# Optimization experiments

Hardware: AMD Instinct MI355X
Metric: run time of the kernel (lower is better)

Reference implementation:

```python
import jax, jax.numpy as jnp
import numpy as np

N_ATOMS = 16384
N_BLOCKS = 4096
K = 3          # top-k nearest context atoms (min(3, n_ctx) in original; n_ctx >> 3 here)
EPS_W = 1e-8   # inverse-distance weight epsilon (matches original)
EPS_D = 1e-12  # tiny epsilon inside sqrt for numerical safety of the distance


def setup_inputs() -> dict:
    key = jax.random.key(0)
    k1, k2, k3, k4, k5 = jax.random.split(key, 5)
    # coordinates spread out like real molecular coords (Angstrom-ish scale)
    X = jax.random.normal(k1, (N_ATOMS, 3), dtype=jnp.float32) * 10.0
    base_noise = jax.random.normal(k2, (N_ATOMS, 3), dtype=jnp.float32)      # randn_like(X)
    centroid_noise = jax.random.normal(k3, (N_ATOMS, 3), dtype=jnp.float32)  # per-atom randn(3)
    block_ids = jnp.sort(jax.random.randint(k4, (N_ATOMS,), 0, N_BLOCKS)).astype(jnp.int32)
    generate_mask = jax.random.randint(k5, (N_BLOCKS,), 0, 2).astype(bool)
    return {
        "X": X,
        "base_noise": base_noise,
        "centroid_noise": centroid_noise,
        "block_ids": block_ids,
        "generate_mask": generate_mask,
    }


def reference(X, base_noise, centroid_noise, block_ids, generate_mask):
    """Vectorized sample_chemical_prior: for every generated atom, find the 3
    nearest CONTEXT atoms, take an inverse-distance-weighted centroid, and add
    0.5 * gaussian noise. Non-generated atoms keep base_noise (randn_like)."""
    n = X.shape[0]
    gen_atoms = generate_mask[block_ids]           # [N] atoms being generated
    ctx = ~gen_atoms                               # [N] context atoms

    # pairwise squared distances via ||a||^2 + ||b||^2 - 2 a.b  -> [N, N]
    xn = jnp.sum(X * X, axis=-1)
    sq = xn[:, None] + xn[None, :] - 2.0 * (X @ X.T)
    d = jnp.sqrt(jnp.maximum(sq, 0.0) + EPS_D)

    # only context atoms are valid neighbor candidates; exclude self for safety
    not_self = ~jnp.eye(n, dtype=bool)
    d = jnp.where(ctx[None, :] & not_self, d, jnp.inf)

    # k nearest context atoms per row (smallest distances)
    neg_dk, idx = jax.lax.top_k(-d, K)             # [N, K]
    dk = -neg_dk

    # inverse-distance weights, normalized (matches original)
    w = 1.0 / (dk + EPS_W)
    w = w / jnp.sum(w, axis=-1, keepdims=True)

    coords = X[idx]                                # [N, K, 3] gather neighbor coords
    centroid = jnp.sum(coords * w[..., None], axis=1)  # [N, 3]

    x0 = jnp.where(gen_atoms[:, None], centroid + 0.5 * centroid_noise, base_noise)
    return x0
```

## Files before the change

kernel.cpp:

```cpp
#include <hip/hip_runtime.h>
#include <cstdint>

#define N_ATOMS 16384
#define NBLK 64
#define NTHR 256
#define G 24
#define NCELLS 13824
#define NCELLS_PAD 14336
#define CPT 14
#define BOX_LO -48.0f
#define INV_CELL 0.25f
#define SINIT 3.0e38f

#define OFF_COUNTS 0
#define OFF_BLKGEN 256
#define OFF_BLKGOFF 512
#define OFF_FLAGS 1024
#define OFF_CNT 3072
#define OFF_START 60416
#define OFF_GENIDX 118016
#define OFF_CTX4 183552

__device__ __forceinline__ int cell1(float x) {
    int c = (int)floorf((x - BOX_LO) * INV_CELL);
    return min(max(c, 0), G - 1);
}

__device__ __forceinline__ void ins3(float v, int vi,
                                     float& s1, float& s2, float& s3,
                                     int& i1, int& i2, int& i3)
{
    const bool b1 = v < s1, b2 = v < s2, b3 = v < s3;
    s3 = b2 ? s2 : (b3 ? v : s3);   i3 = b2 ? i2 : (b3 ? vi : i3);
    s2 = b1 ? s1 : (b2 ? v : s2);   i2 = b1 ? i1 : (b2 ? vi : i2);
    s1 = b1 ? v : s1;               i1 = b1 ? vi : i1;
}

__device__ __forceinline__ void ins3v(float v, float& s1, float& s2, float& s3)
{
    const bool b1 = v < s1, b2 = v < s2, b3 = v < s3;
    s3 = b2 ? s2 : (b3 ? v : s3);
    s2 = b1 ? s1 : (b2 ? v : s2);
    s1 = b1 ? v : s1;
}

__global__ __launch_bounds__(256)
void k0_zero(int4* __restrict__ cell_cnt4)
{
    cell_cnt4[blockIdx.x * 256 + threadIdx.x] = make_int4(0, 0, 0, 0);
}

__global__ __launch_bounds__(NTHR)
void k1_classify(const float* __restrict__ X,
                 const int* __restrict__ block_ids,
                 const unsigned int* __restrict__ mask,
                 const float* __restrict__ base_noise,
                 float* __restrict__ out,
                 unsigned long long* __restrict__ flags,
                 int* __restrict__ blk_gen,
                 int* __restrict__ cell_cnt)
{
    __shared__ int sflag;
    __shared__ int wg[4];
    const int t = threadIdx.x;
    const int wave = t >> 6, lane = t & 63;

    if (t == 0) sflag = 0;
    __syncthreads();
    if (mask[t] > 1u) sflag = 1;
    __syncthreads();
    const bool is_u8 = (sflag != 0);
    const unsigned char* m8 = (const unsigned char*)mask;

    const int i = blockIdx.x * NTHR + t;
    const int bid = block_ids[i];
    const bool g = is_u8 ? (m8[bid] != 0) : (mask[bid] != 0u);

    out[3 * i + 0] = base_noise[3 * i + 0];
    out[3 * i + 1] = base_noise[3 * i + 1];
    out[3 * i + 2] = base_noise[3 * i + 2];

    const unsigned long long mg = __ballot(g);
    if (lane == 0) { flags[blockIdx.x * 4 + wave] = mg; wg[wave] = __popcll(mg); }
    __syncthreads();
    if (t == 0) blk_gen[blockIdx.x] = wg[0] + wg[1] + wg[2] + wg[3];

    if (!g) {
        const float x = X[3 * i], y = X[3 * i + 1], z = X[3 * i + 2];
        const int cx = cell1(x), cy = cell1(y), cz = cell1(z);
        atomicAdd(&cell_cnt[(cz * G + cy) * G + cx], 1);
    }
}

__global__ __launch_bounds__(1024)
void k2_scan(int* __restrict__ cell_cnt,
             int* __restrict__ cell_start,
             const int* __restrict__ blk_gen,
             int* __restrict__ blk_goff,
             int* __restrict__ counts)
{
    const int t = threadIdx.x;
    const int wave = t >> 6, lane = t & 63;
    int loc[CPT]; int sum = 0;
    #pragma unroll
    for (int k = 0; k < CPT; ++k) {
        const int v = cell_cnt[t * CPT + k];
        loc[k] = sum; sum += v;
    }
    int v = sum;
    #pragma unroll
    for (int d = 1; d < 64; d <<= 1) { const int u = __shfl_up(v, d); if (lane >= d) v += u; }
    __shared__ int wsum[16], wexc[16];
    if (lane == 63) wsum[wave] = v;
    __syncthreads();
    if (t < 16) {
        int v2 = wsum[t];
        const int orig = v2;
        #pragma unroll
        for (int d = 1; d < 16; d <<= 1) { const int u = __shfl_up(v2, d); if (t >= d) v2 += u; }
        wexc[t] = v2 - orig;
    }
    __syncthreads();
    const int base = wexc[wave] + (v - sum);
    #pragma unroll
    for (int k = 0; k < CPT; ++k) {
        cell_start[t * CPT + k] = base + loc[k];
        cell_cnt[t * CPT + k] = 0;
    }
    if (t == 1023) cell_start[NCELLS_PAD] = base + sum;
    __syncthreads();
    if (t < 64) {
        const int o = blk_gen[t];
        int s = o;
        #pragma unroll
        for (int d = 1; d < 64; d <<= 1) { const int u = __shfl_up(s, d); if (t >= d) s += u; }
        blk_goff[t] = s - o;
        if (t == 63) { counts[1] = s; counts[0] = N_ATOMS - s; }
    }
}

__global__ __launch_bounds__(NTHR)
void k3_scatter(const float* __restrict__ X,
                const unsigned long long* __restrict__ flags,
                const int* __restrict__ blk_goff,
                const int* __restrict__ cell_start,
                int* __restrict__ cell_cur,
                float4* __restrict__ ctx4s,
                int* __restrict__ genidx)
{
    const int t = threadIdx.x;
    const int wave = t >> 6, lane = t & 63;
    const int i = blockIdx.x * NTHR + t;
    const unsigned long long fw = flags[blockIdx.x * 4 + wave];
    const bool g = (fw >> lane) & 1ull;
    int og = blk_goff[blockIdx.x];
    int oc = blockIdx.x * NTHR - og;
    #pragma unroll
    for (int w = 0; w < 4; ++w) {
        if (w < wave) {
            const int p = __popcll(flags[blockIdx.x * 4 + w]);
            og += p; oc += 64 - p;
        }
    }
    const unsigned long long below = (1ull << lane) - 1ull;
    og += __popcll(fw & below);
    oc += __popcll((~fw) & below);
    if (g) {
        genidx[og] = i;
    } else {
        const float x = X[3 * i], y = X[3 * i + 1], z = X[3 * i + 2];
        float xn = x * x; xn += y * y; xn += z * z;
        const int cx = cell1(x), cy = cell1(y), cz = cell1(z);
        const int c = (cz * G + cy) * G + cx;
        const int pos = cell_start[c] + atomicAdd(&cell_cur[c], 1);
        ctx4s[pos] = make_float4(x, y, z, xn);
    }
}

__global__ __launch_bounds__(512)
void k4_search(const float* __restrict__ X,
               const float* __restrict__ cnoise,
               const int* __restrict__ counts,
               const int* __restrict__ cell_start,
               const float4* __restrict__ ctx4s,
               const int* __restrict__ genidx,
               float* __restrict__ out)
{
    const int n_gen = counts[1];
    const int wave = threadIdx.x >> 6, lane = threadIdx.x & 63;
    const int slot = (int)blockIdx.x * 8 + wave;
    if (slot >= n_gen) return;

    const int ai = genidx[slot];
    const float qx = X[3 * ai], qy = X[3 * ai + 1], qz = X[3 * ai + 2];
    float xnq = qx * qx; xnq += qy * qy; xnq += qz * qz;
    const int cqx = cell1(qx), cqy = cell1(qy), cqz = cell1(qz);

    float s1 = SINIT, s2 = SINIT, s3 = SINIT;
    int i1 = 0, i2 = 0, i3 = 0;

    auto searchOwner = [&](int ebase_r, int jc) -> int {
        int L = 0;
        #pragma unroll
        for (int stp = 32; stp >= 1; stp >>= 1) {
            const int cand = L + stp;
            const int bv = __shfl(ebase_r, cand);
            if (bv <= jc) L = cand;
        }
        return L;
    };

    auto flatScan = [&](int T, int ebase_r, int pk_r) {
        const int iters = (T + 63) >> 6;
        if (iters == 0) return;
        int jc0 = min(lane, T - 1);
        int p0 = __shfl(pk_r, searchOwner(ebase_r, jc0)) + jc0;
        float4 cc0 = ctx4s[p0];
        for (int it = 0; it < iters; ++it) {
            int p1 = p0; float4 cc1 = cc0;
            if (it + 1 < iters) {
                const int jc1 = min((it + 1) * 64 + lane, T - 1);
                p1 = __shfl(pk_r, searchOwner(ebase_r, jc1)) + jc1;
                cc1 = ctx4s[p1];
            }
            if (it * 64 + lane < T) {
                const float dot = qx * cc0.x + qy * cc0.y + qz * cc0.z;
                const float sq = (xnq + cc0.w) - 2.0f * dot;
                ins3(sq, p0, s1, s2, s3, i1, i2, i3);
            }
            p0 = p1; cc0 = cc1;
        }
    };

    auto prefixT = [&](int cnt, int& ebase_r, int& T) {
        int pre = cnt;
        #pragma unroll
        for (int d = 1; d < 64; d <<= 1) {
            const int u = __shfl_up(pre, d);
            if (lane >= d) pre += u;
        }
        T = __shfl(pre, 63);
        ebase_r = pre - cnt;
    };

    auto shellCell = [&](int r, int u, int S, int& st, int& cnt) {
        st = 0; cnt = 0;
        if (u < S) {
            const int B = 2 * r + 1, F = B * B, P8 = 8 * r;
            int dx, dy, dz;
            if (u < 2 * F) {
                dz = (u < F) ? -r : r;
                const int v = (u < F) ? u : u - F;
                dx = v % B - r; dy = v / B - r;
            } else {
                const int v = u - 2 * F;
                dz = v / P8 - (r - 1);
                const int w = v % P8;
                if (w < 2 * r)      { dx = -r + w;          dy = -r; }
                else if (w < 4 * r) { dx = r;               dy = -r + (w - 2 * r); }
                else if (w < 6 * r) { dx = r - (w - 4 * r); dy = r; }
                else                { dx = -r;              dy = r - (w - 6 * r); }
            }
            const int cx = cqx + dx, cy = cqy + dy, cz = cqz + dz;
            if ((unsigned)cx < G && (unsigned)cy < G && (unsigned)cz < G) {
                const int c = (cz * G + cy) * G + cx;
                st = cell_start[c];
                cnt = cell_start[c + 1] - st;
            }
        }
    };

    int cnt = 0, st = 0;
    if (lane < 27) {
        const int dx = lane % 3 - 1, dy = (lane / 3) % 3 - 1, dz = lane / 9 - 1;
        const int cx = cqx + dx, cy = cqy + dy, cz = cqz + dz;
        if ((unsigned)cx < G && (unsigned)cy < G && (unsigned)cz < G) {
            const int c = (cz * G + cy) * G + cx;
            st = cell_start[c];
            cnt = cell_start[c + 1] - st;
        }
    }
    int ebase, T;
    prefixT(cnt, ebase, T);
    flatScan(T, ebase, st - ebase);
    int C = T;
    bool dirty = (T > 0);
    float gm3 = SINIT;

    int r = 1;
    for (;;) {
        if (C >= 3) {
            if (dirty) {
                float m1 = s1, m2 = s2, m3 = s3;
                #pragma unroll
                for (int m = 1; m < 64; m <<= 1) {
                    const float a = __shfl_xor(m1, m);
                    const float b = __shfl_xor(m2, m);
                    const float c = __shfl_xor(m3, m);
                    ins3v(a, m1, m2, m3); ins3v(b, m1, m2, m3); ins3v(c, m1, m2, m3);
                }
                gm3 = m3; dirty = false;
            }
            const float bnd = (float)(4 * r) * (float)(4 * r);
            if (gm3 + 0.01f < bnd) break;
        }
        if (r >= G) break;
        ++r;
        const int S = 24 * r * r + 2;
        const int nro = (S + 63) >> 6;
        int st0, c0;
        shellCell(r, lane, S, st0, c0);
        for (int ro = 0; ro < nro; ++ro) {
            int st1 = st0, c1 = c0;
            if (ro + 1 < nro) shellCell(r, (ro + 1) * 64 + lane, S, st1, c1);
            int eb, Tr;
            prefixT(c0, eb, Tr);
            if (Tr > 0) {
                flatScan(Tr, eb, st0 - eb);
                C += Tr; dirty = true;
            }
            st0 = st1; c0 = c1;
        }
    }

    #pragma unroll
    for (int m = 1; m < 64; m <<= 1) {
        const float a = __shfl_xor(s1, m); const int ja = __shfl_xor(i1, m);
        const float b = __shfl_xor(s2, m); const int jb = __shfl_xor(i2, m);
        const float c = __shfl_xor(s3, m); const int jc = __shfl_xor(i3, m);
        ins3(a, ja, s1, s2, s3, i1, i2, i3);
        ins3(b, jb, s1, s2, s3, i1, i2, i3);
        ins3(c, jc, s1, s2, s3, i1, i2, i3);
    }

    if (lane == 0) {
        const float d1 = sqrtf(fmaxf(s1, 0.0f) + 1e-12f);
        const float d2 = sqrtf(fmaxf(s2, 0.0f) + 1e-12f);
        const float d3 = sqrtf(fmaxf(s3, 0.0f) + 1e-12f);
        float w1 = 1.0f / (d1 + 1e-8f);
        float w2 = 1.0f / (d2 + 1e-8f);
        float w3 = 1.0f / (d3 + 1e-8f);
        float wsum = w1 + w2;
        wsum += w3;
        w1 /= wsum; w2 /= wsum; w3 /= wsum;
        const float4 c1 = ctx4s[i1];
        const float4 c2 = ctx4s[i2];
        const float4 c3 = ctx4s[i3];
        float cxo = w1 * c1.x + w2 * c2.x; cxo += w3 * c3.x;
        float cyo = w1 * c1.y + w2 * c2.y; cyo += w3 * c3.y;
        float czo = w1 * c1.z + w2 * c2.z; czo += w3 * c3.z;
        out[3 * ai + 0] = cxo + 0.5f * cnoise[3 * ai + 0];
        out[3 * ai + 1] = cyo + 0.5f * cnoise[3 * ai + 1];
        out[3 * ai + 2] = czo + 0.5f * cnoise[3 * ai + 2];
    }
}

extern "C" void kernel_launch(void* const* d_in, const int* in_sizes, int n_in,
                              void* d_out, int out_size, void* d_ws, size_t ws_size,
                              hipStream_t stream) {
    const float* X          = (const float*)d_in[0];
    const float* base_noise = (const float*)d_in[1];
    const float* cnoise     = (const float*)d_in[2];
    const int*   block_ids  = (const int*)d_in[3];
    const unsigned int* gmask = (const unsigned int*)d_in[4];
    float* out = (float*)d_out;

    char* ws = (char*)d_ws;
    int*    counts     = (int*)(ws + OFF_COUNTS);
    int*    blk_gen    = (int*)(ws + OFF_BLKGEN);
    int*    blk_goff   = (int*)(ws + OFF_BLKGOFF);
    unsigned long long* flags = (unsigned long long*)(ws + OFF_FLAGS);
    int*    cell_cnt   = (int*)(ws + OFF_CNT);
    int*    cell_start = (int*)(ws + OFF_START);
    int*    genidx     = (int*)(ws + OFF_GENIDX);
    float4* ctx4s      = (float4*)(ws + OFF_CTX4);

    k0_zero<<<NCELLS_PAD / 1024, 256, 0, stream>>>((int4*)cell_cnt);
    k1_classify<<<NBLK, NTHR, 0, stream>>>(X, block_ids, gmask, base_noise,
                                           out, flags, blk_gen, cell_cnt);
    k2_scan<<<1, 1024, 0, stream>>>(cell_cnt, cell_start, blk_gen, blk_goff, counts);
    k3_scatter<<<NBLK, NTHR, 0, stream>>>(X, flags, blk_goff, cell_start,
                                          cell_cnt, ctx4s, genidx);
    k4_search<<<N_ATOMS / 8, 512, 0, stream>>>(X, cnoise, counts, cell_start,
                                               ctx4s, genidx, out);
}
```

Measured before the change: 52.24 us.

## Replace per-cell shell expansion with doubling-radius x-row segment scans

```diff
diff --git a/kernel.cpp b/kernel.cpp
--- a/kernel.cpp
+++ b/kernel.cpp
@@ -243,83 +243,77 @@
         ebase_r = pre - cnt;
     };
 
-    auto shellCell = [&](int r, int u, int S, int& st, int& cnt) {
-        st = 0; cnt = 0;
-        if (u < S) {
-            const int B = 2 * r + 1, F = B * B, P8 = 8 * r;
-            int dx, dy, dz;
-            if (u < 2 * F) {
-                dz = (u < F) ? -r : r;
-                const int v = (u < F) ? u : u - F;
-                dx = v % B - r; dy = v / B - r;
+    auto ringScan = [&](int P, int R) {
+        const int B = 2 * R + 1;
+        const int NR = B * B;
+        const int NS = 2 * NR;
+        auto segRange = [&](int u, int& st, int& cnt) {
+            st = 0; cnt = 0;
+            if (u >= NS) return;
+            const int side = (u >= NR) ? 1 : 0;
+            const int v = side ? u - NR : u;
+            const int dy = v % B - R, dz = v / B - R;
+            const int cy = cqy + dy, cz = cqz + dz;
+            if ((unsigned)cy >= G || (unsigned)cz >= G) return;
+            const bool inner = max(abs(dy), abs(dz)) <= P;
+            int xlo, xhi;
+            if (inner) {
+                if (side) { xlo = cqx + P + 1; xhi = cqx + R; }
+                else      { xlo = cqx - R;     xhi = cqx - P - 1; }
             } else {
-                const int v = u - 2 * F;
-                dz = v / P8 - (r - 1);
-                const int w = v % P8;
-                if (w < 2 * r)      { dx = -r + w;          dy = -r; }
-                else if (w < 4 * r) { dx = r;               dy = -r + (w - 2 * r); }
-                else if (w < 6 * r) { dx = r - (w - 4 * r); dy = r; }
-                else                { dx = -r;              dy = r - (w - 6 * r); }
-            }
-            const int cx = cqx + dx, cy = cqy + dy, cz = cqz + dz;
-            if ((unsigned)cx < G && (unsigned)cy < G && (unsigned)cz < G) {
-                const int c = (cz * G + cy) * G + cx;
-                st = cell_start[c];
-                cnt = cell_start[c + 1] - st;
-            }
+                if (side) return;
+                xlo = cqx - R; xhi = cqx + R;
+            }
+            xlo = max(xlo, 0); xhi = min(xhi, G - 1);
+            if (xlo > xhi) return;
+            const int c0 = (cz * G + cy) * G + xlo;
+            st = cell_start[c0];
+            cnt = cell_start[c0 + (xhi - xlo + 1)] - st;
+        };
+        const int nro = (NS + 63) >> 6;
+        int st0, c0r;
+        segRange(lane, st0, c0r);
+        for (int ro = 0; ro < nro; ++ro) {
+            int st1 = st0, c1r = c0r;
+            if (ro + 1 < nro) segRange((ro + 1) * 64 + lane, st1, c1r);
+            int eb, Tr;
+            prefixT(c0r, eb, Tr);
+            if (Tr > 0) flatScan(Tr, eb, st0 - eb);
+            st0 = st1; c0r = c1r;
         }
     };
 
-    int cnt = 0, st = 0;
-    if (lane < 27) {
-        const int dx = lane % 3 - 1, dy = (lane / 3) % 3 - 1, dz = lane / 9 - 1;
-        const int cx = cqx + dx, cy = cqy + dy, cz = cqz + dz;
-        if ((unsigned)cx < G && (unsigned)cy < G && (unsigned)cz < G) {
-            const int c = (cz * G + cy) * G + cx;
-            st = cell_start[c];
-            cnt = cell_start[c + 1] - st;
-        }
-    }
-    int ebase, T;
-    prefixT(cnt, ebase, T);
-    flatScan(T, ebase, st - ebase);
-    int C = T;
-    bool dirty = (T > 0);
-    float gm3 = SINIT;
-
-    int r = 1;
-    for (;;) {
-        if (C >= 3) {
-            if (dirty) {
-                float m1 = s1, m2 = s2, m3 = s3;
-                #pragma unroll
-                for (int m = 1; m < 64; m <<= 1) {
-                    const float a = __shfl_xor(m1, m);
-                    const float b = __shfl_xor(m2, m);
-                    const float c = __shfl_xor(m3, m);
-                    ins3v(a, m1, m2, m3); ins3v(b, m1, m2, m3); ins3v(c, m1, m2, m3);
-                }
-                gm3 = m3; dirty = false;
-            }
-            const float bnd = (float)(4 * r) * (float)(4 * r);
-            if (gm3 + 0.01f < bnd) break;
-        }
-        if (r >= G) break;
-        ++r;
-        const int S = 24 * r * r + 2;
-        const int nro = (S + 63) >> 6;
-        int st0, c0;
-        shellCell(r, lane, S, st0, c0);
-        for (int ro = 0; ro < nro; ++ro) {
-            int st1 = st0, c1 = c0;
-            if (ro + 1 < nro) shellCell(r, (ro + 1) * 64 + lane, S, st1, c1);
-            int eb, Tr;
-            prefixT(c0, eb, Tr);
-            if (Tr > 0) {
-                flatScan(Tr, eb, st0 - eb);
-                C += Tr; dirty = true;
-            }
-            st0 = st1; c0 = c1;
+    bool done = false;
+    #pragma unroll
+    for (int li = 0; li < 4; ++li) {
+        if (!done) {
+            const int R = 1 << li;
+            const int P = (li == 0) ? -1 : (1 << (li - 1));
+            ringScan(P, R);
+            float m1 = s1, m2 = s2, m3 = s3;
+            #pragma unroll
+            for (int m = 1; m < 64; m <<= 1) {
+                const float a = __shfl_xor(m1, m);
+                const float b = __shfl_xor(m2, m);
+                const float c = __shfl_xor(m3, m);
+                ins3v(a, m1, m2, m3); ins3v(b, m1, m2, m3); ins3v(c, m1, m2, m3);
+            }
+            const float bnd = (float)(4 * R) * (float)(4 * R);
+            if (m3 + 0.01f < bnd) done = true;
+        }
+    }
+    if (!done) {
+        s1 = SINIT; s2 = SINIT; s3 = SINIT;
+        i1 = 0; i2 = 0; i3 = 0;
+        const int n_ctx = counts[0];
+        for (int base = 0; base < n_ctx; base += 64) {
+            const int p = base + lane;
+            if (p < n_ctx) {
+                const float4 cc = ctx4s[p];
+                const float dot = qx * cc.x + qy * cc.y + qz * cc.z;
+                const float sq = (xnq + cc.w) - 2.0f * dot;
+                ins3(sq, p, s1, s2, s3, i1, i2, i3);
+            }
         }
     }
 
```

Result: slower. 54.15 us (+3.7%).
